# Optimization experiments

Hardware: AMD Instinct MI355X
Metric: run time of the kernel (lower is better)

## Reference

```python
import jax, jax.numpy as jnp
import numpy as np

B, C_IN, H, W = 2, 256, 48, 48
OC, G, KH, KW, PH, PW = 256, 4, 7, 7, 3, 3


def _patches(y, Hn, Wn):
    # y: (B, C, Hp, Wp) -> (B, C, KH, KW, Hn, Wn); stride=1, dilation=1
    return jnp.stack([
        jnp.stack([y[:, :, i:i + Hn, j:j + Wn] for j in range(KW)], axis=2)
        for i in range(KH)
    ], axis=2)


def setup_inputs() -> dict:
    key = jax.random.key(0)
    k1, k2, k3, k4 = jax.random.split(key, 4)
    fan_out = 3 * OC  # 1x1 conv, kaiming fan_out
    conv_w = jax.random.normal(k2, (3 * OC, C_IN), dtype=jnp.float32) * np.sqrt(2.0 / fan_out).astype(np.float32)
    return {
        "x": jax.random.normal(k1, (B, C_IN, H, W), dtype=jnp.float32),
        "conv_w": conv_w,
        "rpe_h": jax.random.normal(k3, (G, 1, KH, 1, (OC // G) // 2), dtype=jnp.float32),
        "rpe_w": jax.random.normal(k4, (G, 1, 1, KW, (OC // G) // 2), dtype=jnp.float32),
    }


def reference(x, conv_w, rpe_h, rpe_w):
    b, c, h, w = x.shape
    goc = OC // G
    c2 = goc // 2
    K = KH * KW
    center = (K - 1) // 2
    ci, cj = center // KW, center % KW

    # 1x1 conv to 3*OC channels, then zero-pad (equiv. to Conv2d(padding) + bias=False)
    y = jnp.einsum('bchw,oc->bohw', x, conv_w)
    y = jnp.pad(y, ((0, 0), (0, 0), (PH, PH), (PW, PW)))
    Hn = h + 2 * PH - (KH - 1)
    Wn = w + 2 * PW - (KW - 1)
    P = Hn * Wn

    q_full, k_full, v_full = jnp.split(y, 3, axis=1)

    # query: only the center element of each window is used
    query = q_full[:, :, ci:ci + Hn, cj:cj + Wn].reshape(b, G, goc, P)
    query = jnp.transpose(query, (0, 1, 3, 2))  # (B,G,P,goc)

    # key: full windows + relative position embeddings
    kp = _patches(k_full, Hn, Wn).reshape(b, G, goc, KH, KW, P)
    key = jnp.transpose(kp, (0, 1, 5, 3, 4, 2))  # (B,G,P,KH,KW,goc)
    key = jnp.concatenate((key[..., :c2] + rpe_h, key[..., c2:] + rpe_w), axis=1)  # (B,2G,P,KH,KW,c2)
    key = key.reshape(b, G, P, K, goc)  # row-major reshape matches torch

    vp = _patches(v_full, Hn, Wn).reshape(b, G, goc, K, P)
    value = jnp.transpose(vp, (0, 1, 4, 3, 2))  # (B,G,P,K,goc)

    att = jax.nn.softmax(jnp.einsum('bgpc,bgpkc->bgpk', query, key), axis=-1)
    out = jnp.einsum('bgpk,bgpkc->bgpc', att, value)  # (B,G,P,goc)
    out = jnp.transpose(out, (0, 1, 3, 2)).reshape(b, OC, Hn, Wn)
    return out
```

## Files before the change

### kernel.cpp

```cpp
#include <hip/hip_runtime.h>

#define BB   2
#define CIN  256
#define OC3  768
#define NG   4
#define GOC  64
#define C2   32
#define KK   49
#define PP   2304
#define HALF_P 1152

#define RS      56
#define BROWS   54
#define BSTRIDE (BROWS * RS * OC3)
#define IOFF    ((3 * RS + 3) * OC3)

#define Y2_BYTES  (BB * BROWS * RS * OC3 * 4)
#define XT_OFF    Y2_BYTES
#define WT_OFF    (XT_OFF + BB * PP * 512 * 2)

typedef __attribute__((ext_vector_type(8))) short bf16x8;
typedef __attribute__((ext_vector_type(4))) float f32x4;

struct TagH { static constexpr bool value = true;  };
struct TagW { static constexpr bool value = false; };

static __device__ __forceinline__ unsigned short f2bf_rne(float x) {
    unsigned int u = __float_as_uint(x);
    unsigned int r = u + 0x7FFFu + ((u >> 16) & 1u);
    return (unsigned short)(r >> 16);
}
static __device__ __forceinline__ float bf2f(unsigned short h) {
    return __uint_as_float(((unsigned int)h) << 16);
}

#define ROW4  (RS * OC3 / 4)
#define REG1  (6 * ROW4)
#define COLS4 (OC3 / 4)
__global__ __launch_bounds__(256) void prep(
    const float* __restrict__ X, const float* __restrict__ W,
    float* __restrict__ Y2, short* __restrict__ Xt, short* __restrict__ Wt)
{
    const int bxx = blockIdx.x;
    const int tid = threadIdx.x;
    if (bxx < 1080) {
        const int b   = bxx / 540;
        const int idx = (bxx - b * 540) * 256 + tid;
        float4* Yb = (float4*)(Y2 + (size_t)b * BSTRIDE);
        const float4 z = make_float4(0.f, 0.f, 0.f, 0.f);
        if (idx < REG1) {
            int r6  = idx / ROW4;
            int rem = idx - r6 * ROW4;
            int r   = (r6 < 3) ? r6 : 48 + r6;
            Yb[r * ROW4 + rem] = z;
        } else {
            int i2  = idx - REG1;
            int r   = 3 + i2 / (8 * COLS4);
            int rem = i2 - (r - 3) * (8 * COLS4);
            int cg  = rem / COLS4;
            int c   = (cg < 3) ? cg : 48 + cg;
            int ch4 = rem - cg * COLS4;
            Yb[(r * RS + c) * COLS4 + ch4] = z;
        }
    } else if (bxx < 1848) {
        int t = (bxx - 1080) * 256 + tid;
        int o = t >> 8, c = t & 255;
        float v = W[t];
        unsigned short hi = f2bf_rne(v);
        unsigned short lo = f2bf_rne(v - bf2f(hi));
        Wt[(size_t)o * 512 + c]       = (short)hi;
        Wt[(size_t)o * 512 + 256 + c] = (short)lo;
    } else {
        __shared__ float tile[64][65];
        const int cx = bxx - 1848;
        const int p0 = (cx % 36) * 64;
        const int c0 = ((cx / 36) & 3) * 64;
        const int b  = cx / 144;
        const float* Xb = X + (size_t)b * CIN * PP;
        #pragma unroll
        for (int r = 0; r < 16; ++r) {
            int idx = r * 256 + tid;
            int c = idx >> 6, p = idx & 63;
            tile[c][p] = Xb[(size_t)(c0 + c) * PP + p0 + p];
        }
        __syncthreads();
        short* Xo = Xt + (size_t)b * PP * 512;
        #pragma unroll
        for (int r = 0; r < 16; ++r) {
            int idx = r * 256 + tid;
            int p = idx >> 6, c = idx & 63;
            float v = tile[c][p];
            unsigned short hi = f2bf_rne(v);
            unsigned short lo = f2bf_rne(v - bf2f(hi));
            size_t base = (size_t)(p0 + p) * 512 + c0 + c;
            Xo[base]       = (short)hi;
            Xo[base + 256] = (short)lo;
        }
    }
}

#define LDA 40

__global__ __launch_bounds__(256, 4) void conv_mfma(
    const short* __restrict__ Wt,
    const short* __restrict__ Xt,
    float* __restrict__ Y2)
{
    __shared__ short As[64 * LDA];
    __shared__ short Bs[64 * LDA];

    const int tid = threadIdx.x;
    const int bn  = blockIdx.x;
    const int bm  = blockIdx.y;
    const int b   = blockIdx.z;
    const int om0 = bm * 64, pn0 = bn * 64;

    const int lane = tid & 63, w = tid >> 6;
    const int oq = (w & 1) * 32, pq = (w >> 1) * 32;
    const int ln15 = lane & 15, q = lane >> 4;

    const int  lrow  = (tid & 127) >> 1;
    const int  lsoff = (tid & 1) * 16;
    const bool isA   = tid < 128;
    const short* gA = Wt + (size_t)(om0 + lrow) * 512 + lsoff;
    const short* gB = Xt + (size_t)b * PP * 512 + (size_t)(pn0 + lrow) * 512 + lsoff;
    const short* gsrc = isA ? gA : gB;
    short* ldst = (isA ? As : Bs) + lrow * LDA + lsoff;

    f32x4 acc[2][2] = {};

    for (int k0 = 0; k0 < 768; k0 += 32) {
        const int wk = (k0 < 256) ? k0 : k0 - 256;
        const int xk = (k0 < 512) ? k0 : k0 - 512;
        const int kk = isA ? wk : xk;
        uint4 v0 = *(const uint4*)(gsrc + kk);
        uint4 v1 = *(const uint4*)(gsrc + kk + 8);
        __syncthreads();
        *(uint4*)ldst       = v0;
        *(uint4*)(ldst + 8) = v1;
        __syncthreads();

        bf16x8 af[2], bf[2];
        #pragma unroll
        for (int i = 0; i < 2; ++i) {
            af[i] = *(const bf16x8*)&As[(oq + i * 16 + ln15) * LDA + q * 8];
            bf[i] = *(const bf16x8*)&Bs[(pq + i * 16 + ln15) * LDA + q * 8];
        }
        #pragma unroll
        for (int i = 0; i < 2; ++i)
            #pragma unroll
            for (int j = 0; j < 2; ++j)
                acc[i][j] = __builtin_amdgcn_mfma_f32_16x16x32_bf16(
                    af[i], bf[j], acc[i][j], 0, 0, 0);
    }

    float* Yb = Y2 + (size_t)b * BSTRIDE + IOFF;
    #pragma unroll
    for (int i = 0; i < 2; ++i) {
        #pragma unroll
        for (int j = 0; j < 2; ++j) {
            int o = om0 + oq + i * 16 + q * 4;
            int p = pn0 + pq + j * 16 + ln15;
            int h = p / 48, ww = p - h * 48;
            *(f32x4*)&Yb[(size_t)(h * RS + ww) * OC3 + o] = acc[i][j];
        }
    }
}

__global__ __launch_bounds__(256, 4) void attn_kernel(
    const float* __restrict__ Y2,
    const float* __restrict__ rpe_h,
    const float* __restrict__ rpe_w,
    float* __restrict__ out)
{
    __shared__ float Ks[7 * 14 * 32];
    __shared__ float Vs[7 * 10 * 64];
    __shared__ float Qs[4 * 64];
    __shared__ float xpose[4][65];

    const int tid  = threadIdx.x;
    const int lane = tid & 63;
    const int w    = tid >> 6;
    const int bx     = blockIdx.x;
    const int wblock = (bx & 7) * 576 + (bx >> 3);
    const int wid0   = wblock * 4;
    const int pq0  = wid0 % PP;
    const int g    = (wid0 / PP) & (NG - 1);
    const int b    = wid0 / (PP * NG);
    const int ph   = pq0 / 48;
    const int pws  = pq0 - ph * 48;
    const int t    = (pq0 >= HALF_P) ? 1 : 0;
    const int qp0  = pq0 - t * HALF_P;
    const int p00  = 2 * qp0;
    const int ph0  = p00 / 48;
    const int w0   = p00 - ph0 * 48;
    const int g2   = 2 * g + t;
    const bool use_h = (g2 < NG);
    const int  kch   = use_h ? (CIN + g2 * GOC) : (CIN + (g2 - NG) * GOC + C2);
    const int  vch   = 2 * CIN + g * GOC;

    const float* Yb = Y2 + (size_t)b * BSTRIDE + IOFF;

    #pragma unroll
    for (int it = 0; it < 8; ++it) {
        int idx = it * 256 + tid;
        if (idx < 784) {
            int run = idx >> 3, f4o = idx & 7;
            int row = run / 14, col = run - row * 14;
            const float* src = Yb + (long)((ph0 + row - 3) * RS + (w0 + col - 3)) * OC3
                               + kch + f4o * 4;
            *(float4*)&Ks[run * 32 + f4o * 4] = *(const float4*)src;
        } else if (idx < 1904) {
            int r = idx - 784;
            int run = r >> 4, f4o = r & 15;
            int row = run / 10, col = run - row * 10;
            const float* src = Yb + (long)((ph + row - 3) * RS + (pws + col - 3)) * OC3
                               + vch + f4o * 4;
            *(float4*)&Vs[run * 64 + f4o * 4] = *(const float4*)src;
        } else if (idx < 1968) {
            int r = idx - 1904;
            int pi = r >> 4, f4o = r & 15;
            const float* src = Yb + (long)(ph * RS + pws + pi) * OC3 + g * GOC + f4o * 4;
            *(float4*)&Qs[pi * 64 + f4o * 4] = *(const float4*)src;
        }
    }

    const int  c  = lane & 31;
    const bool hi = (lane >= 32);
    const float* rb = use_h ? (rpe_h + g2 * 7 * C2) : (rpe_w + (g2 - NG) * 7 * C2);
    const float R0 = rb[0 * C2 + c], R1 = rb[1 * C2 + c], R2 = rb[2 * C2 + c],
                R3 = rb[3 * C2 + c], R4 = rb[4 * C2 + c], R5 = rb[5 * C2 + c],
                R6 = rb[6 * C2 + c];

    __syncthreads();

    const float qv = Qs[w * GOC + lane];
    const float* kls = Ks + w * 64 + c;
    const float* vls = Vs + w * 64 + lane;

    auto rget = [&](int idx) -> float {
        return idx == 0 ? R0 : idx == 1 ? R1 : idx == 2 ? R2 :
               idx == 3 ? R3 : idx == 4 ? R4 : idx == 5 ? R5 : R6;
    };

    auto tree = [&](auto tag) -> float {
        constexpr bool UH = decltype(tag)::value;
        auto chunkprod = [&](int l) -> float {
            int m0 = 2 * l,     h10 = (m0 >= KK), k0 = m0 - KK * h10;
            int m1 = 2 * l + 1, h11 = (m1 >= KK), k1 = m1 - KK * h11;
            int i0 = k0 / 7, j0 = k0 % 7, i1 = k1 / 7, j1 = k1 % 7;
            int d0 = (i0 * 14 + j0 + h10) * 32;
            int d1 = (i1 * 14 + j1 + h11) * 32;
            float kv = kls[hi ? d1 : d0];
            float ra = UH ? rget(i0) : rget(j0);
            float rc = UH ? rget(i1) : rget(j1);
            kv += hi ? rc : ra;
            return qv * kv;
        };
        float sv[32];
        #pragma unroll
        for (int jj = 0; jj < 32; ++jj) {
            if (2 * jj >= KK) { sv[jj] = 0.f; continue; }
            float pa = chunkprod(2 * jj);
            float pb = (2 * jj + 1 < KK) ? chunkprod(2 * jj + 1) : 0.f;
            float u  = (lane & 1) ? pb : pa;
            float ww = (lane & 1) ? pa : pb;
            sv[jj] = u + __shfl_xor(ww, 1, 64);
        }
        #pragma unroll
        for (int d = 2; d < 64; d <<= 1) {
            #pragma unroll
            for (int i = 0; i < 32; i += d) {
                float a  = sv[i], bb = sv[i + d / 2];
                float u  = (lane & d) ? bb : a;
                float ww = (lane & d) ? a : bb;
                sv[i] = u + __shfl_xor(ww, d, 64);
            }
        }
        return sv[0];
    };

    const float logit = use_h ? tree(TagH{}) : tree(TagW{});

    float mx = logit;
    #pragma unroll
    for (int d = 1; d < 64; d <<= 1)
        mx = fmaxf(mx, __shfl_xor(mx, d, 64));
    float e = (lane < KK) ? __expf(logit - mx) : 0.f;
    float ssum = e;
    #pragma unroll
    for (int d = 1; d < 64; d <<= 1)
        ssum += __shfl_xor(ssum, d, 64);
    const float att = e / ssum;

    float acc = 0.f;
    #pragma unroll
    for (int k = 0; k < KK; ++k) {
        int i = k / 7, j = k % 7;
        float ak = __uint_as_float(
            __builtin_amdgcn_readlane(__float_as_uint(att), k));
        acc = fmaf(ak, vls[(i * 10 + j) * 64], acc);
    }

    xpose[w][lane] = acc;
    __syncthreads();
    const int ch = tid >> 2;
    const int w2 = tid & 3;
    out[((size_t)b * 256 + g * GOC + ch) * PP + pq0 + w2] = xpose[w2][ch];
}

extern "C" void kernel_launch(void* const* d_in, const int* in_sizes, int n_in,
                              void* d_out, int out_size, void* d_ws, size_t ws_size,
                              hipStream_t stream)
{
    const float* x  = (const float*)d_in[0];
    const float* w  = (const float*)d_in[1];
    const float* rh = (const float*)d_in[2];
    const float* rw = (const float*)d_in[3];

    float* Y2 = (float*)d_ws;
    short* Xt = (short*)((char*)d_ws + XT_OFF);
    short* Wt = (short*)((char*)d_ws + WT_OFF);

    prep<<<2136, 256, 0, stream>>>(x, w, Y2, Xt, Wt);
    conv_mfma<<<dim3(36, 12, BB), 256, 0, stream>>>(Wt, Xt, Y2);
    attn_kernel<<<(BB * NG * PP) / 4, 256, 0, stream>>>(Y2, rh, rw, (float*)d_out);
}
```

Baseline: 123.2 us.

## Restructure attention logits with vectorized dot products, DPP reductions, direct V loads

```diff
diff --git a/kernel.cpp b/kernel.cpp
--- a/kernel.cpp
+++ b/kernel.cpp
@@ -32,6 +32,12 @@
 }
 static __device__ __forceinline__ float bf2f(unsigned short h) {
     return __uint_as_float(((unsigned int)h) << 16);
+}
+
+template<int CTRL>
+static __device__ __forceinline__ float dpp_mov_f(float x) {
+    return __int_as_float(__builtin_amdgcn_update_dpp(
+        0, __float_as_int(x), CTRL, 0xF, 0xF, true));
 }
 
 #define ROW4  (RS * OC3 / 4)
@@ -167,15 +173,14 @@
     }
 }
 
+#define KSTR 36
 __global__ __launch_bounds__(256, 4) void attn_kernel(
     const float* __restrict__ Y2,
     const float* __restrict__ rpe_h,
     const float* __restrict__ rpe_w,
     float* __restrict__ out)
 {
-    __shared__ float Ks[7 * 14 * 32];
-    __shared__ float Vs[7 * 10 * 64];
-    __shared__ float Qs[4 * 64];
+    __shared__ float Ks[98 * KSTR];
     __shared__ float xpose[4][65];
 
     const int tid  = threadIdx.x;
@@ -202,104 +207,105 @@
     const float* Yb = Y2 + (size_t)b * BSTRIDE + IOFF;
 
     #pragma unroll
-    for (int it = 0; it < 8; ++it) {
+    for (int it = 0; it < 4; ++it) {
         int idx = it * 256 + tid;
         if (idx < 784) {
             int run = idx >> 3, f4o = idx & 7;
             int row = run / 14, col = run - row * 14;
             const float* src = Yb + (long)((ph0 + row - 3) * RS + (w0 + col - 3)) * OC3
                                + kch + f4o * 4;
-            *(float4*)&Ks[run * 32 + f4o * 4] = *(const float4*)src;
-        } else if (idx < 1904) {
-            int r = idx - 784;
-            int run = r >> 4, f4o = r & 15;
-            int row = run / 10, col = run - row * 10;
-            const float* src = Yb + (long)((ph + row - 3) * RS + (pws + col - 3)) * OC3
-                               + vch + f4o * 4;
-            *(float4*)&Vs[run * 64 + f4o * 4] = *(const float4*)src;
-        } else if (idx < 1968) {
-            int r = idx - 1904;
-            int pi = r >> 4, f4o = r & 15;
-            const float* src = Yb + (long)(ph * RS + pws + pi) * OC3 + g * GOC + f4o * 4;
-            *(float4*)&Qs[pi * 64 + f4o * 4] = *(const float4*)src;
-        }
-    }
-
-    const int  c  = lane & 31;
-    const bool hi = (lane >= 32);
+            *(float4*)&Ks[run * KSTR + f4o * 4] = *(const float4*)src;
+        }
+    }
+
+    const int tsub = lane >> 3;
+    const int cq   = lane & 7;
+
+    const float* qbase = Yb + (long)(ph * RS + pws + w) * OC3 + g * GOC;
+    const float4 qlo = *(const float4*)(qbase + 4 * cq);
+    const float4 qhi = *(const float4*)(qbase + 32 + 4 * cq);
+
     const float* rb = use_h ? (rpe_h + g2 * 7 * C2) : (rpe_w + (g2 - NG) * 7 * C2);
-    const float R0 = rb[0 * C2 + c], R1 = rb[1 * C2 + c], R2 = rb[2 * C2 + c],
-                R3 = rb[3 * C2 + c], R4 = rb[4 * C2 + c], R5 = rb[5 * C2 + c],
-                R6 = rb[6 * C2 + c];
+    float A0, A1, A2, A3, A4, A5, A6, H0, H1, H2, H3, H4, H5, H6;
+    {
+        auto rl = [&](int r, float& Ar, float& Hr) {
+            float4 v = *(const float4*)(rb + r * 32 + 4 * cq);
+            Ar = qlo.x * v.x + qlo.y * v.y + qlo.z * v.z + qlo.w * v.w;
+            Hr = qhi.x * v.x + qhi.y * v.y + qhi.z * v.z + qhi.w * v.w;
+        };
+        rl(0, A0, H0); rl(1, A1, H1); rl(2, A2, H2); rl(3, A3, H3);
+        rl(4, A4, H4); rl(5, A5, H5); rl(6, A6, H6);
+    }
+    auto selA = [&](int i) -> float {
+        return i == 0 ? A0 : i == 1 ? A1 : i == 2 ? A2 :
+               i == 3 ? A3 : i == 4 ? A4 : i == 5 ? A5 : A6;
+    };
+    auto selH = [&](int i) -> float {
+        return i == 0 ? H0 : i == 1 ? H1 : i == 2 ? H2 :
+               i == 3 ? H3 : i == 4 ? H4 : i == 5 ? H5 : H6;
+    };
 
     __syncthreads();
 
-    const float qv = Qs[w * GOC + lane];
-    const float* kls = Ks + w * 64 + c;
-    const float* vls = Vs + w * 64 + lane;
-
-    auto rget = [&](int idx) -> float {
-        return idx == 0 ? R0 : idx == 1 ? R1 : idx == 2 ? R2 :
-               idx == 3 ? R3 : idx == 4 ? R4 : idx == 5 ? R5 : R6;
+    auto logits = [&](auto tag) -> float {
+        constexpr bool UH = decltype(tag)::value;
+        float lg = 0.f;
+        #pragma unroll
+        for (int l = 0; l < 7; ++l) {
+            int kp = 8 * l + tsub;
+            int m0 = 2 * kp, m1 = m0 + 1;
+            int h10 = (m0 >= KK) ? 1 : 0; int k0 = m0 - KK * h10;
+            int h11 = (m1 >= KK) ? 1 : 0; int k1 = m1 - KK * h11;
+            int i0 = (k0 * 37) >> 8; int j0 = k0 - 7 * i0;
+            int i1 = (k1 * 37) >> 8; int j1 = k1 - 7 * i1;
+            int offA = (i0 * 14 + 2 * w + j0 + h10) * KSTR + 4 * cq;
+            int offB = (i1 * 14 + 2 * w + j1 + h11) * KSTR + 4 * cq;
+            offA = min(offA, 98 * KSTR - 4);
+            offB = min(offB, 98 * KSTR - 4);
+            float4 ka = *(const float4*)&Ks[offA];
+            float4 kb = *(const float4*)&Ks[offB];
+            float part = qlo.x * ka.x + qlo.y * ka.y + qlo.z * ka.z + qlo.w * ka.w
+                       + qhi.x * kb.x + qhi.y * kb.y + qhi.z * kb.z + qhi.w * kb.w
+                       + (UH ? selA(i0) : selA(j0))
+                       + (UH ? selH(i1) : selH(j1));
+            part += dpp_mov_f<0xB1>(part);
+            part += dpp_mov_f<0x4E>(part);
+            part += dpp_mov_f<0x141>(part);
+            if (l == 6) part = (tsub == 0) ? part : 0.f;
+            lg = (cq == l) ? part : lg;
+        }
+        return lg;
     };
-
-    auto tree = [&](auto tag) -> float {
-        constexpr bool UH = decltype(tag)::value;
-        auto chunkprod = [&](int l) -> float {
-            int m0 = 2 * l,     h10 = (m0 >= KK), k0 = m0 - KK * h10;
-            int m1 = 2 * l + 1, h11 = (m1 >= KK), k1 = m1 - KK * h11;
-            int i0 = k0 / 7, j0 = k0 % 7, i1 = k1 / 7, j1 = k1 % 7;
-            int d0 = (i0 * 14 + j0 + h10) * 32;
-            int d1 = (i1 * 14 + j1 + h11) * 32;
-            float kv = kls[hi ? d1 : d0];
-            float ra = UH ? rget(i0) : rget(j0);
-            float rc = UH ? rget(i1) : rget(j1);
-            kv += hi ? rc : ra;
-            return qv * kv;
-        };
-        float sv[32];
-        #pragma unroll
-        for (int jj = 0; jj < 32; ++jj) {
-            if (2 * jj >= KK) { sv[jj] = 0.f; continue; }
-            float pa = chunkprod(2 * jj);
-            float pb = (2 * jj + 1 < KK) ? chunkprod(2 * jj + 1) : 0.f;
-            float u  = (lane & 1) ? pb : pa;
-            float ww = (lane & 1) ? pa : pb;
-            sv[jj] = u + __shfl_xor(ww, 1, 64);
-        }
-        #pragma unroll
-        for (int d = 2; d < 64; d <<= 1) {
-            #pragma unroll
-            for (int i = 0; i < 32; i += d) {
-                float a  = sv[i], bb = sv[i + d / 2];
-                float u  = (lane & d) ? bb : a;
-                float ww = (lane & d) ? a : bb;
-                sv[i] = u + __shfl_xor(ww, d, 64);
-            }
-        }
-        return sv[0];
-    };
-
-    const float logit = use_h ? tree(TagH{}) : tree(TagW{});
+    const float logit = use_h ? logits(TagH{}) : logits(TagW{});
 
     float mx = logit;
-    #pragma unroll
-    for (int d = 1; d < 64; d <<= 1)
-        mx = fmaxf(mx, __shfl_xor(mx, d, 64));
-    float e = (lane < KK) ? __expf(logit - mx) : 0.f;
+    mx = fmaxf(mx, dpp_mov_f<0xB1>(mx));
+    mx = fmaxf(mx, dpp_mov_f<0x4E>(mx));
+    mx = fmaxf(mx, dpp_mov_f<0x141>(mx));
+    mx = fmaxf(mx, dpp_mov_f<0x128>(mx));
+    mx = fmaxf(mx, __shfl_xor(mx, 16, 64));
+    mx = fmaxf(mx, __shfl_xor(mx, 32, 64));
+    const int Lx = 8 * cq + tsub;
+    float e = (Lx < KK) ? __expf(logit - mx) : 0.f;
     float ssum = e;
-    #pragma unroll
-    for (int d = 1; d < 64; d <<= 1)
-        ssum += __shfl_xor(ssum, d, 64);
+    ssum += dpp_mov_f<0xB1>(ssum);
+    ssum += dpp_mov_f<0x4E>(ssum);
+    ssum += dpp_mov_f<0x141>(ssum);
+    ssum += dpp_mov_f<0x128>(ssum);
+    ssum += __shfl_xor(ssum, 16, 64);
+    ssum += __shfl_xor(ssum, 32, 64);
     const float att = e / ssum;
 
     float acc = 0.f;
+    const float* vb = Yb + (long)(ph * RS + pws + w) * OC3 + vch + lane;
     #pragma unroll
     for (int k = 0; k < KK; ++k) {
         int i = k / 7, j = k % 7;
+        int doff = ((i - 3) * RS + (j - 3)) * OC3;
+        int src  = 8 * (k & 7) + (k >> 3);
         float ak = __uint_as_float(
-            __builtin_amdgcn_readlane(__float_as_uint(att), k));
-        acc = fmaf(ak, vls[(i * 10 + j) * 64], acc);
+            __builtin_amdgcn_readlane(__float_as_uint(att), src));
+        acc = fmaf(ak, vb[doff], acc);
     }
 
     xpose[w][lane] = acc;
```

After: 119.7 us. 2.9% less time.
